# Performance work log

Hardware: AMD Instinct MI355X
Metric: run time of the kernel (lower is better)

## Reference

```python
import jax, jax.numpy as jnp
import numpy as np

K = 1024          # num_embeddings
D = 128           # embedding_dim
COMMITMENT_COST = 0.25


def setup_inputs() -> dict:
    key = jax.random.key(0)
    k1, k2 = jax.random.split(key)
    inputs = jax.random.normal(k1, (16, D, 4096), dtype=jnp.float32)
    codebook = jax.random.normal(k2, (K, D), dtype=jnp.float32)
    return {"inputs": inputs, "codebook": codebook}


def reference(inputs, codebook):
    # inputs: [B, D, T]; codebook: [K, D]
    B, Dd, T = inputs.shape
    flat = jnp.transpose(inputs, (0, 2, 1)).reshape(-1, Dd)  # [N, D], N = B*T
    N = flat.shape[0]

    d = (jnp.sum(flat * flat, axis=1, keepdims=True)
         + jnp.sum(codebook * codebook, axis=1)
         - 2.0 * flat @ codebook.T)
    idx = jnp.argmin(d, axis=1)  # [N]

    # gather-based quantization (same math as one-hot @ codebook)
    quantized = codebook[idx]                                   # [N, D]
    quantized = quantized.reshape(B, T, Dd).transpose(0, 2, 1)  # [B, D, T]

    # commitment loss (quantized detached; stop_gradient irrelevant in fwd)
    e_latent_loss = jnp.mean((jax.lax.stop_gradient(quantized) - inputs) ** 2)
    loss = COMMITMENT_COST * e_latent_loss

    # straight-through estimator
    quantized_st = inputs + jax.lax.stop_gradient(quantized - inputs)

    # perplexity from code usage histogram (= mean of one-hot encodings)
    counts = jnp.zeros((codebook.shape[0],), dtype=jnp.float32).at[idx].add(1.0)
    avg_probs = counts / N
    perplexity = jnp.exp(-jnp.sum(avg_probs * jnp.log(avg_probs + 1e-10)))

    return loss, quantized_st, perplexity, idx.reshape(B, T)
```

## Files before the change

### kernel.cpp

```cpp
#include <hip/hip_runtime.h>

#define T_FULL 4096
#define D 128
#define K 1024
#define NVEC 65536
#define BDT 8388608
#define BT 128
#define NBLK (NVEC / BT)
#define KT 32
#define NIT (K / KT)
#define PLANE_B (K * D * 2)
#define TILE_B (2 * KT * D * 2)
#define TPLANE (KT * D * 2)
#define GTILE (KT * D * 2)

typedef _Float16 f16x8 __attribute__((ext_vector_type(8)));
typedef float f32x4 __attribute__((ext_vector_type(4)));

#define MFMA(a, b, c) __builtin_amdgcn_mfma_f32_16x16x32_f16((a), (b), (c), 0, 0, 0)

#define GLOAD_LDS(g, l)                                                        \
  __builtin_amdgcn_global_load_lds(                                            \
      (const __attribute__((address_space(1))) unsigned int*)(g),              \
      (__attribute__((address_space(3))) unsigned int*)(l), 16, 0, 0)

__global__ __launch_bounds__(128) void prep_kernel(const float* __restrict__ cb,
    float* __restrict__ ee, _Float16* __restrict__ E1, _Float16* __restrict__ E2,
    unsigned int* __restrict__ counts, unsigned int* __restrict__ done,
    float* __restrict__ loss_acc) {
  int k = blockIdx.x, d = threadIdx.x;
  if (d == 0) {
    counts[k] = 0u;
    if (k == 0) { *done = 0u; *loss_acc = 0.f; }
  }
  float e = cb[k * D + d];
  float v = e * e;
#pragma unroll
  for (int o = 32; o > 0; o >>= 1) v += __shfl_down(v, o, 64);
  __shared__ float tmp[2];
  if ((d & 63) == 0) tmp[d >> 6] = v;
  __syncthreads();
  if (d == 0) ee[k] = tmp[0] + tmp[1];

  float s = 2.0f * e;
  _Float16 h1 = (_Float16)s;
  _Float16 h2 = (_Float16)(s - (float)h1);
  E1[k * D + d] = h1;
  E2[k * D + d] = h2;
}

__global__ __launch_bounds__(256, 2) void vq_main(
    const float* __restrict__ inp, const float* __restrict__ cb,
    const float* __restrict__ ee, const _Float16* __restrict__ Eplanes,
    unsigned int* __restrict__ counts, unsigned int* __restrict__ done,
    float* __restrict__ loss_acc, float* __restrict__ out) {
  __shared__ __align__(16) _Float16 Bs[2 * 2 * KT * D + 4096];
  __shared__ float ee_sh[K];
  __shared__ int   midx[BT];
  __shared__ float lred[4];
  __shared__ int   lastf;

  float* out_q   = out + 1;
  float* out_idx = out + 2 + BDT;

  const int tid  = threadIdx.x;
  const int lane = tid & 63;
  const int w    = tid >> 6;
  const int c    = lane & 15;
  const int q    = lane >> 4;
  const int b    = blockIdx.x >> 5;
  const int t0   = (blockIdx.x & 31) * BT;

  unsigned soff[4], slds[4];
#pragma unroll
  for (int i = 0; i < 4; ++i) {
    int flat = tid + i * 256;
    int p    = flat >> 9;
    int s    = flat & 511;
    int code = s >> 4;
    int dgp  = s & 15;
    int dg   = dgp ^ (code & 15);
    soff[i] = (unsigned)(p * PLANE_B + code * 256 + dg * 16);
    slds[i] = (unsigned)(flat * 16);
  }
  const char* Eb = (const char*)Eplanes;

#pragma unroll
  for (int i = 0; i < 4; ++i)
    GLOAD_LDS(Eb + soff[i], (char*)Bs + slds[i]);

  f16x8 A1[2][4], A2[2][4];
  {
    const float* xin = inp + (size_t)b * D * T_FULL + t0 + w * 32 + c;
#pragma unroll
    for (int n = 0; n < 2; ++n)
#pragma unroll
      for (int dc = 0; dc < 4; ++dc) {
        f16x8 a1, a2;
#pragma unroll
        for (int j = 0; j < 8; ++j) {
          int d = dc * 32 + q * 8 + j;
          float x = xin[(size_t)d * T_FULL + n * 16];
          _Float16 h1 = (_Float16)x;
          _Float16 h2 = (_Float16)(x - (float)h1);
          a1[j] = h1; a2[j] = h2;
        }
        A1[n][dc] = a1; A2[n][dc] = a2;
      }
  }
#pragma unroll
  for (int i = tid; i < K; i += 256) ee_sh[i] = ee[i];
  __syncthreads();

  float bv[2][4];
  int   bi[2][4];
#pragma unroll
  for (int n = 0; n < 2; ++n)
#pragma unroll
    for (int r = 0; r < 4; ++r) { bv[n][r] = 3.4e38f; bi[n][r] = 0; }

  for (int it = 0; it < NIT; ++it) {
    const int kt = it * KT;
    const int bb = it & 1;

    if (it) __syncthreads();

    if (it != NIT - 1) {
      const char* gs = Eb + (size_t)(it + 1) * GTILE;
      const unsigned lbo = (unsigned)((bb ^ 1) * TILE_B);
#pragma unroll
      for (int i = 0; i < 4; ++i)
        GLOAD_LDS(gs + soff[i], (char*)Bs + lbo + slds[i]);
    }

    f32x4 accM[2][2], accC[2][2];
#pragma unroll
    for (int n = 0; n < 2; ++n)
#pragma unroll
      for (int kf = 0; kf < 2; ++kf) {
        accM[n][kf] = (f32x4){0.f, 0.f, 0.f, 0.f};
        accC[n][kf] = (f32x4){0.f, 0.f, 0.f, 0.f};
      }

    const char* Bp = (const char*)Bs + bb * TILE_B;
#pragma unroll
    for (int dc = 0; dc < 4; ++dc) {
      const int sw = ((dc * 4 + q) ^ c) * 16;
      f16x8 B1[2], B2[2];
#pragma unroll
      for (int kf = 0; kf < 2; ++kf) {
        const int ro = (kf * 16 + c) * 256 + sw;
        B1[kf] = *(const f16x8*)(Bp + ro);
        B2[kf] = *(const f16x8*)(Bp + TPLANE + ro);
      }
#pragma unroll
      for (int n = 0; n < 2; ++n)
#pragma unroll
        for (int kf = 0; kf < 2; ++kf) {
          accM[n][kf] = MFMA(A1[n][dc], B1[kf], accM[n][kf]);
          f32x4 t_ = accC[n][kf];
          t_ = MFMA(A1[n][dc], B2[kf], t_);
          t_ = MFMA(A2[n][dc], B1[kf], t_);
          accC[n][kf] = t_;
        }
    }

#pragma unroll
    for (int kf = 0; kf < 2; ++kf) {
      const int code = kt + kf * 16 + c;
      const float eev = ee_sh[code];
#pragma unroll
      for (int n = 0; n < 2; ++n)
#pragma unroll
        for (int r = 0; r < 4; ++r) {
          float dist = eev - accM[n][kf][r] - accC[n][kf][r];
          if (dist < bv[n][r]) { bv[n][r] = dist; bi[n][r] = code; }
        }
    }
  }

#pragma unroll
  for (int m = 1; m <= 8; m <<= 1)
#pragma unroll
    for (int n = 0; n < 2; ++n)
#pragma unroll
      for (int r = 0; r < 4; ++r) {
        float ov = __shfl_xor(bv[n][r], m, 64);
        int   oi = __shfl_xor(bi[n][r], m, 64);
        if (ov < bv[n][r] || (ov == bv[n][r] && oi < bi[n][r])) {
          bv[n][r] = ov; bi[n][r] = oi;
        }
      }
  if (c == 0) {
#pragma unroll
    for (int n = 0; n < 2; ++n)
#pragma unroll
      for (int r = 0; r < 4; ++r)
        midx[w * 32 + n * 16 + q * 4 + r] = bi[n][r];
  }
  __syncthreads();

  if (tid < BT) {
    int ki = midx[tid];
    out_idx[(size_t)b * T_FULL + t0 + tid] = (float)ki;
    atomicAdd(&counts[ki], 1u);
  }

  float lsum = 0.f;
  {
    const int t  = tid & 127;
    const int dh = tid >> 7;
    const int kq = midx[t];
    const float* crow = cb + (size_t)kq * D + dh * 64;
    const float* xrow = inp + ((size_t)b * D + dh * 64) * T_FULL + t0 + t;
    float*       qrow = out_q + ((size_t)b * D + dh * 64) * T_FULL + t0 + t;
#pragma unroll
    for (int dd = 0; dd < 64; dd += 4) {
      float4 qv = *(const float4*)(crow + dd);
      float x0 = xrow[(size_t)(dd + 0) * T_FULL];
      float x1 = xrow[(size_t)(dd + 1) * T_FULL];
      float x2 = xrow[(size_t)(dd + 2) * T_FULL];
      float x3 = xrow[(size_t)(dd + 3) * T_FULL];
      float df;
      df = qv.x - x0; lsum = fmaf(df, df, lsum); qrow[(size_t)(dd + 0) * T_FULL] = qv.x;
      df = qv.y - x1; lsum = fmaf(df, df, lsum); qrow[(size_t)(dd + 1) * T_FULL] = qv.y;
      df = qv.z - x2; lsum = fmaf(df, df, lsum); qrow[(size_t)(dd + 2) * T_FULL] = qv.z;
      df = qv.w - x3; lsum = fmaf(df, df, lsum); qrow[(size_t)(dd + 3) * T_FULL] = qv.w;
    }
  }
#pragma unroll
  for (int o = 32; o > 0; o >>= 1) lsum += __shfl_down(lsum, o, 64);
  if (lane == 0) lred[w] = lsum;
  __syncthreads();
  if (tid == 0) {
    atomicAdd(loss_acc, lred[0] + lred[1] + lred[2] + lred[3]);
    __threadfence();
    unsigned ticket = atomicAdd(done, 1u);
    lastf = (ticket == NBLK - 1) ? 1 : 0;
  }
  __syncthreads();

  if (lastf) {
    __threadfence();
    float ent = 0.f;
#pragma unroll
    for (int i = tid; i < K; i += 256) {
      float cnt = (float)atomicAdd(&counts[i], 0u);
      float p = cnt * (1.0f / (float)NVEC);
      ent = fmaf(p, logf(p + 1e-10f), ent);
    }
#pragma unroll
    for (int o = 32; o > 0; o >>= 1) ent += __shfl_down(ent, o, 64);
    if (lane == 0) lred[w] = ent;
    __syncthreads();
    if (tid == 0) {
      float e = lred[0] + lred[1] + lred[2] + lred[3];
      float l = atomicAdd(loss_acc, 0.f);
      out[0]       = 0.25f * (l / (float)BDT);
      out[1 + BDT] = expf(-e);
    }
  }
}

extern "C" void kernel_launch(void* const* d_in, const int* in_sizes, int n_in,
                              void* d_out, int out_size, void* d_ws, size_t ws_size,
                              hipStream_t stream) {
  const float* inp = (const float*)d_in[0];
  const float* cb  = (const float*)d_in[1];
  float* out = (float*)d_out;

  char* ws = (char*)d_ws;
  unsigned int* counts  = (unsigned int*)ws;
  unsigned int* done    = (unsigned int*)(ws + 4096);
  float*        lossacc = (float*)(ws + 4160);
  float*        ee      = (float*)(ws + 8192);
  _Float16*     E1      = (_Float16*)(ws + 12288);
  _Float16*     E2      = (_Float16*)(ws + 12288 + PLANE_B);

  prep_kernel<<<K, 128, 0, stream>>>(cb, ee, E1, E2, counts, done, lossacc);
  vq_main<<<NBLK, 256, 0, stream>>>(inp, cb, ee, E1, counts, done, lossacc, out);
}
```

Before: 189.2 us.

## Split codebook search across wave pairs with smaller token tiles and merged accumulator

Halves tokens per block to 64 and splits the 1024-code search into two halves, one per wave pair, each streaming its own 16-code tiles into separate LDS double buffers. The two halves' argmin results are merged through shared memory. The separate main and correction accumulators are fused into a single MFMA chain, and occupancy is set via waves_per_eu(4,4). This doubles the grid and shrinks per-thread register state to raise occupancy, at the cost of more blocks re-reading inputs and codebook tiles, and of ties between the two halves resolving slightly differently.

New measurement: 207.3 us. 1.1x slower.

```diff
diff --git a/kernel.cpp b/kernel.cpp
--- a/kernel.cpp
+++ b/kernel.cpp
@@ -5,12 +5,13 @@
 #define K 1024
 #define NVEC 65536
 #define BDT 8388608
-#define BT 128
+#define BT 64
 #define NBLK (NVEC / BT)
-#define KT 32
-#define NIT (K / KT)
+#define KH 512
+#define KT 16
+#define NIT (KH / KT)
 #define PLANE_B (K * D * 2)
-#define TILE_B (2 * KT * D * 2)
+#define HTILE_B (2 * KT * D * 2)
 #define TPLANE (KT * D * 2)
 #define GTILE (KT * D * 2)
 
@@ -49,13 +50,17 @@
   E2[k * D + d] = h2;
 }
 
-__global__ __launch_bounds__(256, 2) void vq_main(
+__global__ __launch_bounds__(256)
+__attribute__((amdgpu_waves_per_eu(4, 4)))
+void vq_main(
     const float* __restrict__ inp, const float* __restrict__ cb,
     const float* __restrict__ ee, const _Float16* __restrict__ Eplanes,
     unsigned int* __restrict__ counts, unsigned int* __restrict__ done,
     float* __restrict__ loss_acc, float* __restrict__ out) {
-  __shared__ __align__(16) _Float16 Bs[2 * 2 * KT * D + 4096];
+  __shared__ __align__(16) _Float16 Bs[2 * 2 * KT * D * 2];
   __shared__ float ee_sh[K];
+  __shared__ float mval[2][BT];
+  __shared__ int   mi[2][BT];
   __shared__ int   midx[BT];
   __shared__ float lred[4];
   __shared__ int   lastf;
@@ -66,32 +71,37 @@
   const int tid  = threadIdx.x;
   const int lane = tid & 63;
   const int w    = tid >> 6;
+  const int h    = w >> 1;
+  const int tw   = (w & 1) * 32;
   const int c    = lane & 15;
   const int q    = lane >> 4;
-  const int b    = blockIdx.x >> 5;
-  const int t0   = (blockIdx.x & 31) * BT;
-
+  const int b    = blockIdx.x >> 6;
+  const int t0   = (blockIdx.x & 63) * BT;
+  const int k0   = h * KH;
+
+  const int ptid = tid & 127;
   unsigned soff[4], slds[4];
 #pragma unroll
   for (int i = 0; i < 4; ++i) {
-    int flat = tid + i * 256;
-    int p    = flat >> 9;
-    int s    = flat & 511;
+    int flat = ptid + i * 128;
+    int p    = flat >> 8;
+    int s    = flat & 255;
     int code = s >> 4;
     int dgp  = s & 15;
-    int dg   = dgp ^ (code & 15);
+    int dg   = dgp ^ code;
     soff[i] = (unsigned)(p * PLANE_B + code * 256 + dg * 16);
     slds[i] = (unsigned)(flat * 16);
   }
-  const char* Eb = (const char*)Eplanes;
+  const char* Eb = (const char*)Eplanes + (size_t)k0 * 256;
+  char* BsH = (char*)Bs + h * (2 * HTILE_B);
 
 #pragma unroll
   for (int i = 0; i < 4; ++i)
-    GLOAD_LDS(Eb + soff[i], (char*)Bs + slds[i]);
+    GLOAD_LDS(Eb + soff[i], BsH + slds[i]);
 
   f16x8 A1[2][4], A2[2][4];
   {
-    const float* xin = inp + (size_t)b * D * T_FULL + t0 + w * 32 + c;
+    const float* xin = inp + (size_t)b * D * T_FULL + t0 + tw + c;
 #pragma unroll
     for (int n = 0; n < 2; ++n)
 #pragma unroll
@@ -120,63 +130,48 @@
     for (int r = 0; r < 4; ++r) { bv[n][r] = 3.4e38f; bi[n][r] = 0; }
 
   for (int it = 0; it < NIT; ++it) {
-    const int kt = it * KT;
     const int bb = it & 1;
 
     if (it) __syncthreads();
 
     if (it != NIT - 1) {
       const char* gs = Eb + (size_t)(it + 1) * GTILE;
-      const unsigned lbo = (unsigned)((bb ^ 1) * TILE_B);
+      char* ld = BsH + (bb ^ 1) * HTILE_B;
 #pragma unroll
       for (int i = 0; i < 4; ++i)
-        GLOAD_LDS(gs + soff[i], (char*)Bs + lbo + slds[i]);
-    }
-
-    f32x4 accM[2][2], accC[2][2];
-#pragma unroll
-    for (int n = 0; n < 2; ++n)
-#pragma unroll
-      for (int kf = 0; kf < 2; ++kf) {
-        accM[n][kf] = (f32x4){0.f, 0.f, 0.f, 0.f};
-        accC[n][kf] = (f32x4){0.f, 0.f, 0.f, 0.f};
-      }
-
-    const char* Bp = (const char*)Bs + bb * TILE_B;
+        GLOAD_LDS(gs + soff[i], ld + slds[i]);
+    }
+
+    f32x4 acc[2];
+    acc[0] = (f32x4){0.f, 0.f, 0.f, 0.f};
+    acc[1] = (f32x4){0.f, 0.f, 0.f, 0.f};
+
+    const char* Bp = BsH + bb * HTILE_B;
 #pragma unroll
     for (int dc = 0; dc < 4; ++dc) {
       const int sw = ((dc * 4 + q) ^ c) * 16;
-      f16x8 B1[2], B2[2];
-#pragma unroll
-      for (int kf = 0; kf < 2; ++kf) {
-        const int ro = (kf * 16 + c) * 256 + sw;
-        B1[kf] = *(const f16x8*)(Bp + ro);
-        B2[kf] = *(const f16x8*)(Bp + TPLANE + ro);
-      }
-#pragma unroll
-      for (int n = 0; n < 2; ++n)
-#pragma unroll
-        for (int kf = 0; kf < 2; ++kf) {
-          accM[n][kf] = MFMA(A1[n][dc], B1[kf], accM[n][kf]);
-          f32x4 t_ = accC[n][kf];
-          t_ = MFMA(A1[n][dc], B2[kf], t_);
-          t_ = MFMA(A2[n][dc], B1[kf], t_);
-          accC[n][kf] = t_;
-        }
-    }
-
-#pragma unroll
-    for (int kf = 0; kf < 2; ++kf) {
-      const int code = kt + kf * 16 + c;
-      const float eev = ee_sh[code];
-#pragma unroll
-      for (int n = 0; n < 2; ++n)
-#pragma unroll
-        for (int r = 0; r < 4; ++r) {
-          float dist = eev - accM[n][kf][r] - accC[n][kf][r];
-          if (dist < bv[n][r]) { bv[n][r] = dist; bi[n][r] = code; }
-        }
-    }
+      const int ro = c * 256 + sw;
+      f16x8 B1 = *(const f16x8*)(Bp + ro);
+      f16x8 B2 = *(const f16x8*)(Bp + TPLANE + ro);
+#pragma unroll
+      for (int n = 0; n < 2; ++n) {
+        f32x4 a = acc[n];
+        a = MFMA(A1[n][dc], B1, a);
+        a = MFMA(A1[n][dc], B2, a);
+        a = MFMA(A2[n][dc], B1, a);
+        acc[n] = a;
+      }
+    }
+
+    const int code = k0 + it * KT + c;
+    const float eev = ee_sh[code];
+#pragma unroll
+    for (int n = 0; n < 2; ++n)
+#pragma unroll
+      for (int r = 0; r < 4; ++r) {
+        float dist = eev - acc[n][r];
+        if (dist < bv[n][r]) { bv[n][r] = dist; bi[n][r] = code; }
+      }
   }
 
 #pragma unroll
@@ -195,27 +190,33 @@
 #pragma unroll
     for (int n = 0; n < 2; ++n)
 #pragma unroll
-      for (int r = 0; r < 4; ++r)
-        midx[w * 32 + n * 16 + q * 4 + r] = bi[n][r];
+      for (int r = 0; r < 4; ++r) {
+        const int t = tw + n * 16 + q * 4 + r;
+        mval[h][t] = bv[n][r];
+        mi[h][t]   = bi[n][r];
+      }
   }
   __syncthreads();
 
   if (tid < BT) {
-    int ki = midx[tid];
+    float v0 = mval[0][tid], v1 = mval[1][tid];
+    int   ki = (v1 < v0) ? mi[1][tid] : mi[0][tid];
+    midx[tid] = ki;
     out_idx[(size_t)b * T_FULL + t0 + tid] = (float)ki;
     atomicAdd(&counts[ki], 1u);
   }
+  __syncthreads();
 
   float lsum = 0.f;
   {
-    const int t  = tid & 127;
-    const int dh = tid >> 7;
+    const int t  = tid & 63;
+    const int dq = tid >> 6;
     const int kq = midx[t];
-    const float* crow = cb + (size_t)kq * D + dh * 64;
-    const float* xrow = inp + ((size_t)b * D + dh * 64) * T_FULL + t0 + t;
-    float*       qrow = out_q + ((size_t)b * D + dh * 64) * T_FULL + t0 + t;
-#pragma unroll
-    for (int dd = 0; dd < 64; dd += 4) {
+    const float* crow = cb + (size_t)kq * D + dq * 32;
+    const float* xrow = inp + ((size_t)b * D + dq * 32) * T_FULL + t0 + t;
+    float*       qrow = out_q + ((size_t)b * D + dq * 32) * T_FULL + t0 + t;
+#pragma unroll
+    for (int dd = 0; dd < 32; dd += 4) {
       float4 qv = *(const float4*)(crow + dd);
       float x0 = xrow[(size_t)(dd + 0) * T_FULL];
       float x1 = xrow[(size_t)(dd + 1) * T_FULL];
```
